# Performance work log

Measured on AMD Instinct MI355X. Metric: run time of the kernel, lower is better.

## Reference

```python
import jax, jax.numpy as jnp
import numpy as np

EMBED_DIM = 1024
HEADS = 16
D_HEAD = EMBED_DIM // HEADS
B, S = 4, 2048


def setup_inputs() -> dict:
    key = jax.random.key(0)
    ks = jax.random.split(key, 7)
    scale = 1.0 / np.sqrt(EMBED_DIM)
    inp = {
        "key": jax.random.normal(ks[0], (B, S, EMBED_DIM), jnp.float32),
        "query": jax.random.normal(ks[1], (B, S, EMBED_DIM), jnp.float32),
        "value": jax.random.normal(ks[2], (B, S, EMBED_DIM), jnp.float32),
        # causal boolean mask, broadcastable to [B, H, S, S]
        "mask": jnp.tril(jnp.ones((S, S), dtype=bool))[None, None, :, :] * jnp.ones((B, 1, 1, 1), dtype=bool),
        # nn.Linear weights, stored torch-style as [out_features, in_features]
        "Wq": jax.random.normal(ks[3], (EMBED_DIM, EMBED_DIM), jnp.float32) * scale,
        "Wk": jax.random.normal(ks[4], (EMBED_DIM, EMBED_DIM), jnp.float32) * scale,
        "Wv": jax.random.normal(ks[5], (EMBED_DIM, EMBED_DIM), jnp.float32) * scale,
        "Wo": jax.random.normal(ks[6], (EMBED_DIM, EMBED_DIM), jnp.float32) * scale,
    }
    return inp


def reference(key, query, value, mask, Wq, Wk, Wv, Wo):
    # projections (nn.Linear, bias=False): x @ W.T
    q = query @ Wq.T                                    # [B,S,E]
    k = key @ Wk.T
    v = value @ Wv.T
    # split heads -> [B,H,S,d]
    def split(x):
        return x.reshape(B, S, HEADS, D_HEAD).transpose(0, 2, 1, 3)
    q, k, v = split(q), split(k), split(v)
    # scaled dot-product scores [B,H,S,S]
    scores = jnp.einsum("bhqd,bhkd->bhqk", q, k) / np.sqrt(D_HEAD).astype(np.float32)
    scores = jnp.where(mask, scores, jnp.float32(-1e9))
    attn = jax.nn.softmax(scores, axis=-1)
    # attention output, merge heads
    out = jnp.einsum("bhqk,bhkd->bhqd", attn, v)        # [B,H,S,d]
    out = out.transpose(0, 2, 1, 3).reshape(B, S, EMBED_DIM)
    return out @ Wo.T
```

## Files before the change

### kernel.cpp

```cpp
#include <hip/hip_runtime.h>

#define SEQ 2048
#define EMBED 1024
#define DHEAD 64

typedef _Float16 h8 __attribute__((ext_vector_type(8)));
typedef _Float16 h4 __attribute__((ext_vector_type(4)));
typedef float f4 __attribute__((ext_vector_type(4)));
typedef unsigned int u32;

__device__ __forceinline__ void gload_lds16(const void* g, void* l) {
    __builtin_amdgcn_global_load_lds(
        (const __attribute__((address_space(1))) u32*)g,
        (__attribute__((address_space(3))) u32*)l, 16, 0, 0);
}

__device__ __forceinline__ h8 cvt8(f4 a, f4 b) {
    return (h8){ (_Float16)a[0], (_Float16)a[1], (_Float16)a[2], (_Float16)a[3],
                 (_Float16)b[0], (_Float16)b[1], (_Float16)b[2], (_Float16)b[3] };
}

__global__ __launch_bounds__(256) void cvt_w(
    const float* __restrict__ wq, const float* __restrict__ wk,
    const float* __restrict__ wv, const float* __restrict__ wo,
    _Float16* __restrict__ wq16, _Float16* __restrict__ wk16,
    _Float16* __restrict__ wv16, _Float16* __restrict__ wo16)
{
    int bid = blockIdx.x;
    int seg = bid >> 10;
    size_t base = (size_t)(bid & 1023) * 1024 + threadIdx.x * 4;
    const float* src = seg == 0 ? wq : seg == 1 ? wk : seg == 2 ? wv : wo;
    _Float16* dst = seg == 0 ? wq16 : seg == 1 ? wk16 : seg == 2 ? wv16 : wo16;
    float scale = (seg == 0) ? 0.18033688011112042f : 1.0f;
    float4 x = *(const float4*)(src + base);
    h4 y = { (_Float16)(x.x * scale), (_Float16)(x.y * scale),
             (_Float16)(x.z * scale), (_Float16)(x.w * scale) };
    *(h4*)(dst + base) = y;
}

template <bool A32, bool B32>
__device__ __forceinline__ void gemm_core_t(const void* Ap, const void* Wp,
                                            int m0, int n0, int tid,
                                            _Float16* As, _Float16* Bs, f4 acc[4][4])
{
    const int lane = tid & 63, wave = tid >> 6;
    const int t16 = lane & 15, quad = lane >> 4;
    const int wm = (wave >> 1) * 64, wn = (wave & 1) * 64;
    const int r0 = tid >> 2;
    const int c0 = (tid & 3) * 8;

    for (int k0 = 0; k0 < 1024; k0 += 32) {
        __syncthreads();
        f4 xa0, xa1, xa2, xa3, xb0, xb1, xb2, xb3;
        if constexpr (A32) {
            const float* ga = (const float*)Ap + (size_t)(m0 + r0) * 1024 + c0 + k0;
            xa0 = *(const f4*)ga;       xa1 = *(const f4*)(ga + 4);
            xa2 = *(const f4*)(ga + 65536); xa3 = *(const f4*)(ga + 65536 + 4);
        }
        if constexpr (B32) {
            const float* gb = (const float*)Wp + (size_t)(n0 + r0) * 1024 + c0 + k0;
            xb0 = *(const f4*)gb;       xb1 = *(const f4*)(gb + 4);
            xb2 = *(const f4*)(gb + 65536); xb3 = *(const f4*)(gb + 65536 + 4);
        }
        if constexpr (!A32) {
            const _Float16* ga = (const _Float16*)Ap + (size_t)(m0 + r0) * 1024 + c0 + k0;
            gload_lds16(ga, As + wave * 512);
            gload_lds16(ga + (size_t)64 * 1024, As + 2048 + wave * 512);
        }
        if constexpr (!B32) {
            const _Float16* gb = (const _Float16*)Wp + (size_t)(n0 + r0) * 1024 + c0 + k0;
            gload_lds16(gb, Bs + wave * 512);
            gload_lds16(gb + (size_t)64 * 1024, Bs + 2048 + wave * 512);
        }
        if constexpr (A32) {
            *(h8*)(As + tid * 8) = cvt8(xa0, xa1);
            *(h8*)(As + 2048 + tid * 8) = cvt8(xa2, xa3);
        }
        if constexpr (B32) {
            *(h8*)(Bs + tid * 8) = cvt8(xb0, xb1);
            *(h8*)(Bs + 2048 + tid * 8) = cvt8(xb2, xb3);
        }
        __syncthreads();
        h8 af[4], bf[4];
#pragma unroll
        for (int i = 0; i < 4; ++i)
            af[i] = *(const h8*)(As + (wm + i * 16 + t16) * 32 + quad * 8);
#pragma unroll
        for (int j = 0; j < 4; ++j)
            bf[j] = *(const h8*)(Bs + (wn + j * 16 + t16) * 32 + quad * 8);
#pragma unroll
        for (int i = 0; i < 4; ++i)
#pragma unroll
            for (int j = 0; j < 4; ++j)
                acc[i][j] = __builtin_amdgcn_mfma_f32_16x16x32_f16(af[i], bf[j], acc[i][j], 0, 0, 0);
    }
}

__global__ __launch_bounds__(256) void proj_qkv(
    const float* __restrict__ qf, const float* __restrict__ kf, const float* __restrict__ vf,
    const _Float16* __restrict__ Wq, const _Float16* __restrict__ Wk, const _Float16* __restrict__ Wv,
    _Float16* __restrict__ Qh, _Float16* __restrict__ Kh, _Float16* __restrict__ Vt)
{
    __shared__ _Float16 As[4096], Bs[4096];
    const int tid = threadIdx.x;
    const int z = blockIdx.z;
    int m0, n0;
    f4 acc[4][4];
    const f4 z4 = {0.f, 0.f, 0.f, 0.f};
#pragma unroll
    for (int i = 0; i < 4; ++i)
#pragma unroll
        for (int j = 0; j < 4; ++j) acc[i][j] = z4;

    if (z == 2) {
        m0 = blockIdx.y * 128; n0 = blockIdx.x * 128;
        gemm_core_t<false, true>(Wv, vf, m0, n0, tid, As, Bs, acc);
    } else if (z == 0) {
        m0 = blockIdx.x * 128; n0 = blockIdx.y * 128;
        gemm_core_t<true, false>(qf, Wq, m0, n0, tid, As, Bs, acc);
    } else {
        m0 = blockIdx.x * 128; n0 = blockIdx.y * 128;
        gemm_core_t<true, false>(kf, Wk, m0, n0, tid, As, Bs, acc);
    }

    const int lane = tid & 63, wave = tid >> 6;
    const int t16 = lane & 15, quad = lane >> 4;
    const int wm = (wave >> 1) * 64, wn = (wave & 1) * 64;
#pragma unroll
    for (int i = 0; i < 4; ++i)
#pragma unroll
        for (int j = 0; j < 4; ++j)
#pragma unroll
            for (int reg = 0; reg < 4; ++reg) {
                int gm = m0 + wm + i * 16 + quad * 4 + reg;
                int gn = n0 + wn + j * 16 + t16;
                float vv = acc[i][j][reg];
                if (z < 2) {
                    int b = gm >> 11, s = gm & 2047, h = gn >> 6, dd = gn & 63;
                    _Float16* dst = (z == 0) ? Qh : Kh;
                    dst[(((size_t)(b * 16 + h) * SEQ) + s) * DHEAD + dd] = (_Float16)vv;
                } else {
                    int h = gm >> 6, dd = gm & 63, b = gn >> 11, s = gn & 2047;
                    int jt = s >> 6, ks = s & 63;
                    int j4 = ks >> 4, quadv = (ks >> 2) & 3, regv = ks & 3;
                    int dt = dd >> 4, t16v = dd & 15;
                    size_t off = (size_t)(b * 16 + h) * (SEQ * DHEAD)
                               + (size_t)(jt * 8 + dt * 2 + (j4 >> 1)) * 512
                               + (quadv * 16 + t16v) * 8 + (j4 & 1) * 4 + regv;
                    Vt[off] = (_Float16)vv;
                }
            }
}

__global__ __launch_bounds__(256) void attn3(
    const _Float16* __restrict__ Qh, const _Float16* __restrict__ Kh,
    const _Float16* __restrict__ Vt, _Float16* __restrict__ Ob)
{
    __shared__ _Float16 Kbuf[2][8][512];
    __shared__ _Float16 Vbuf[2][8][512];

    const int tid = threadIdx.x;
    const int lane = tid & 63, wave = tid >> 6;
    const int t16 = lane & 15, quad = lane >> 4;
    const int bh = blockIdx.x;
    const int b = bh >> 4, h = bh & 15;
    const int qb = (gridDim.y - 1) - blockIdx.y;
    const int q0 = qb * 128;
    const int nqt = qb * 2 + 2;

    const _Float16* Qp = Qh + (size_t)bh * SEQ * DHEAD;
    const _Float16* Kp = Kh + (size_t)bh * SEQ * DHEAD;
    const _Float16* Vp = Vt + (size_t)bh * SEQ * DHEAD;

    const int qlo[2] = { q0 + wave * 32, q0 + wave * 32 + 16 };
    const int last0 = (qlo[0] + 15) >> 6;

    h8 qf[2][2];
#pragma unroll
    for (int qb2 = 0; qb2 < 2; ++qb2)
#pragma unroll
        for (int kc = 0; kc < 2; ++kc)
            qf[qb2][kc] = *(const h8*)(Qp + (size_t)(qlo[qb2] + t16) * 64 + kc * 32 + quad * 8);

    const _Float16* Kl = Kp + t16 * 64 + quad * 8;
    const _Float16* Vl = Vp + lane * 8;

#define STAGE(jt_, bufi)                                                                  \
    do {                                                                                  \
        if (wave < 2) {                                                                   \
            _Pragma("unroll")                                                             \
            for (int i_ = 0; i_ < 4; ++i_) {                                              \
                int g_ = wave * 4 + i_;                                                   \
                gload_lds16(Kl + (jt_) * 4096 + (g_ >> 1) * 1024 + (g_ & 1) * 32,         \
                            &Kbuf[bufi][g_][0]);                                          \
            }                                                                             \
        } else {                                                                          \
            _Pragma("unroll")                                                             \
            for (int i_ = 0; i_ < 4; ++i_) {                                              \
                int g_ = (wave - 2) * 4 + i_;                                             \
                gload_lds16(Vl + ((jt_) * 8 + g_) * 512, &Vbuf[bufi][g_][0]);             \
            }                                                                             \
        }                                                                                 \
    } while (0)

    STAGE(0, 0);
    __syncthreads();

    float mv[2] = {-1e30f, -1e30f};
    float lv[2] = {0.f, 0.f};
    f4 o_acc[2][4];
    const f4 z4 = {0.f, 0.f, 0.f, 0.f};
#pragma unroll
    for (int qb2 = 0; qb2 < 2; ++qb2)
#pragma unroll
        for (int dt = 0; dt < 4; ++dt) o_acc[qb2][dt] = z4;

    for (int jt = 0; jt < nqt; ++jt) {
        const int buf = jt & 1;
        if (jt + 1 < nqt) STAGE(jt + 1, buf ^ 1);

        if (jt <= last0) {
            f4 s0[4], s1[4];
#pragma unroll
            for (int j4 = 0; j4 < 4; ++j4) {
                h8 kfa = *(const h8*)(&Kbuf[buf][j4 * 2 + 0][lane * 8]);
                h8 kfb = *(const h8*)(&Kbuf[buf][j4 * 2 + 1][lane * 8]);
                s1[j4] = __builtin_amdgcn_mfma_f32_16x16x32_f16(kfa, qf[1][0], z4, 0, 0, 0);
                s1[j4] = __builtin_amdgcn_mfma_f32_16x16x32_f16(kfb, qf[1][1], s1[j4], 0, 0, 0);
                s0[j4] = __builtin_amdgcn_mfma_f32_16x16x32_f16(kfa, qf[0][0], z4, 0, 0, 0);
                s0[j4] = __builtin_amdgcn_mfma_f32_16x16x32_f16(kfb, qf[0][1], s0[j4], 0, 0, 0);
            }

            h4 pf0[4], pf1[4];
            auto softmax_frag = [&](f4* s, int qb2, h4* pf) {
                const int myq = qlo[qb2] + t16;
                if ((jt << 6) + 63 > qlo[qb2]) {
#pragma unroll
                    for (int j4 = 0; j4 < 4; ++j4)
#pragma unroll
                        for (int reg = 0; reg < 4; ++reg) {
                            int kk = (jt << 6) + j4 * 16 + quad * 4 + reg;
                            if (kk > myq) s[j4][reg] = -1e30f;
                        }
                }
                float mr = s[0][0];
#pragma unroll
                for (int j4 = 0; j4 < 4; ++j4)
#pragma unroll
                    for (int reg = 0; reg < 4; ++reg) mr = fmaxf(mr, s[j4][reg]);
                mr = fmaxf(mr, __shfl_xor(mr, 16, 64));
                mr = fmaxf(mr, __shfl_xor(mr, 32, 64));
                float mn = mv[qb2];
                if (__any(mr > mn + 8.0f)) {
                    mn = fmaxf(mn, mr);
                    float al = __builtin_amdgcn_exp2f(mv[qb2] - mn);
                    mv[qb2] = mn;
                    lv[qb2] *= al;
#pragma unroll
                    for (int dt = 0; dt < 4; ++dt)
#pragma unroll
                        for (int reg = 0; reg < 4; ++reg) o_acc[qb2][dt][reg] *= al;
                }
                float rs = 0.f;
#pragma unroll
                for (int j4 = 0; j4 < 4; ++j4) {
#pragma unroll
                    for (int reg = 0; reg < 4; ++reg) {
                        float p = __builtin_amdgcn_exp2f(s[j4][reg] - mn);
                        s[j4][reg] = p;
                        rs += p;
                    }
                    pf[j4] = (h4){ (_Float16)s[j4][0], (_Float16)s[j4][1],
                                   (_Float16)s[j4][2], (_Float16)s[j4][3] };
                }
                rs += __shfl_xor(rs, 16, 64);
                rs += __shfl_xor(rs, 32, 64);
                lv[qb2] += rs;
            };
            softmax_frag(s0, 0, pf0);
            softmax_frag(s1, 1, pf1);

#pragma unroll
            for (int dt = 0; dt < 4; ++dt) {
#pragma unroll
                for (int j4p = 0; j4p < 2; ++j4p) {
                    h8 v2 = *(const h8*)(&Vbuf[buf][dt * 2 + j4p][lane * 8]);
                    h4 vlo = __builtin_shufflevector(v2, v2, 0, 1, 2, 3);
                    h4 vhi = __builtin_shufflevector(v2, v2, 4, 5, 6, 7);
                    o_acc[0][dt] = __builtin_amdgcn_mfma_f32_16x16x16f16(vlo, pf0[j4p * 2 + 0], o_acc[0][dt], 0, 0, 0);
                    o_acc[0][dt] = __builtin_amdgcn_mfma_f32_16x16x16f16(vhi, pf0[j4p * 2 + 1], o_acc[0][dt], 0, 0, 0);
                    o_acc[1][dt] = __builtin_amdgcn_mfma_f32_16x16x16f16(vlo, pf1[j4p * 2 + 0], o_acc[1][dt], 0, 0, 0);
                    o_acc[1][dt] = __builtin_amdgcn_mfma_f32_16x16x16f16(vhi, pf1[j4p * 2 + 1], o_acc[1][dt], 0, 0, 0);
                }
            }
        }
        __syncthreads();
    }

    _Float16* ep = ((_Float16*)Kbuf) + wave * 1024;
    const int swz = (t16 & 7) << 3;
#pragma unroll
    for (int qb2 = 0; qb2 < 2; ++qb2) {
        float inv = __builtin_amdgcn_rcpf(lv[qb2]);
#pragma unroll
        for (int dt = 0; dt < 4; ++dt) {
            h4 ov = { (_Float16)(o_acc[qb2][dt][0] * inv), (_Float16)(o_acc[qb2][dt][1] * inv),
                      (_Float16)(o_acc[qb2][dt][2] * inv), (_Float16)(o_acc[qb2][dt][3] * inv) };
            *(h4*)(ep + t16 * 64 + ((dt * 16 + quad * 4) ^ swz)) = ov;
        }
        h8 r0 = *(const h8*)(ep + t16 * 64 + ((quad * 8) ^ swz));
        h8 r1 = *(const h8*)(ep + t16 * 64 + ((32 + quad * 8) ^ swz));
        int s = qlo[qb2] + t16;
        _Float16* og = Ob + ((size_t)(b * SEQ + s)) * EMBED + h * DHEAD;
        *(h8*)(og + quad * 8) = r0;
        *(h8*)(og + 32 + quad * 8) = r1;
    }
#undef STAGE
}

__global__ __launch_bounds__(256) void proj_out(
    const _Float16* __restrict__ A, const _Float16* __restrict__ Wo, float* __restrict__ out)
{
    __shared__ _Float16 As[4096], Bs[4096];
    const int tid = threadIdx.x;
    const int m0 = blockIdx.x * 128, n0 = blockIdx.y * 128;
    f4 acc[4][4];
    const f4 z4 = {0.f, 0.f, 0.f, 0.f};
#pragma unroll
    for (int i = 0; i < 4; ++i)
#pragma unroll
        for (int j = 0; j < 4; ++j) acc[i][j] = z4;

    gemm_core_t<false, false>(A, Wo, m0, n0, tid, As, Bs, acc);

    const int lane = tid & 63, wave = tid >> 6;
    const int t16 = lane & 15, quad = lane >> 4;
    const int wm = (wave >> 1) * 64, wn = (wave & 1) * 64;
#pragma unroll
    for (int i = 0; i < 4; ++i)
#pragma unroll
        for (int j = 0; j < 4; ++j)
#pragma unroll
            for (int reg = 0; reg < 4; ++reg) {
                int gm = m0 + wm + i * 16 + quad * 4 + reg;
                int gn = n0 + wn + j * 16 + t16;
                out[(size_t)gm * EMBED + gn] = acc[i][j][reg];
            }
}

extern "C" void kernel_launch(void* const* d_in, const int* in_sizes, int n_in,
                              void* d_out, int out_size, void* d_ws, size_t ws_size,
                              hipStream_t stream) {
    const float* key   = (const float*)d_in[0];
    const float* query = (const float*)d_in[1];
    const float* value = (const float*)d_in[2];
    const float* Wq = (const float*)d_in[4];
    const float* Wk = (const float*)d_in[5];
    const float* Wv = (const float*)d_in[6];
    const float* Wo = (const float*)d_in[7];

    char* ws = (char*)d_ws;
    _Float16* Ob   = (_Float16*)(ws);
    _Float16* Wq16 = (_Float16*)(ws + (16u << 20));
    _Float16* Wk16 = (_Float16*)(ws + (18u << 20));
    _Float16* Wv16 = (_Float16*)(ws + (20u << 20));
    _Float16* Wo16 = (_Float16*)(ws + (22u << 20));
    _Float16* Qh   = (_Float16*)(ws + (24u << 20));
    _Float16* Kh   = (_Float16*)(ws + (40u << 20));
    _Float16* Vt   = (_Float16*)(ws + (56u << 20));

    dim3 blk(256);
    cvt_w<<<dim3(4096), blk, 0, stream>>>(Wq, Wk, Wv, Wo, Wq16, Wk16, Wv16, Wo16);
    proj_qkv<<<dim3(64, 8, 3), blk, 0, stream>>>(query, key, value, Wq16, Wk16, Wv16, Qh, Kh, Vt);
    attn3<<<dim3(64, 16), blk, 0, stream>>>(Qh, Kh, Vt, Ob);
    proj_out<<<dim3(64, 8), blk, 0, stream>>>(Ob, Wo16, (float*)d_out);
}
```

Before: 364.9 us.

## Double-buffer LDS tiles in projection GEMM core to overlap loads with MFMA

Restructures the shared GEMM core used by the QKV and output projections into a two-stage pipeline. The next K-slice's global loads (direct-to-LDS for fp16, register prefetch for fp32) are issued before the current slice's MFMAs, and there is now one barrier per iteration instead of two. This is meant to hide global load latency behind compute. In exchange, LDS per block doubles to 32KB and fp32 operands stay live in registers across the MFMA section, which may reduce occupancy.

```diff
diff --git a/kernel.cpp b/kernel.cpp
--- a/kernel.cpp
+++ b/kernel.cpp
@@ -49,50 +49,74 @@
     const int r0 = tid >> 2;
     const int c0 = (tid & 3) * 8;
 
-    for (int k0 = 0; k0 < 1024; k0 += 32) {
-        __syncthreads();
-        f4 xa0, xa1, xa2, xa3, xb0, xb1, xb2, xb3;
+    f4 xa0, xa1, xa2, xa3, xb0, xb1, xb2, xb3;
+
+    auto loadA = [&](int k0, int bf) {
         if constexpr (A32) {
             const float* ga = (const float*)Ap + (size_t)(m0 + r0) * 1024 + c0 + k0;
-            xa0 = *(const f4*)ga;       xa1 = *(const f4*)(ga + 4);
+            xa0 = *(const f4*)ga;           xa1 = *(const f4*)(ga + 4);
             xa2 = *(const f4*)(ga + 65536); xa3 = *(const f4*)(ga + 65536 + 4);
-        }
+        } else {
+            const _Float16* ga = (const _Float16*)Ap + (size_t)(m0 + r0) * 1024 + c0 + k0;
+            gload_lds16(ga, As + bf * 4096 + wave * 512);
+            gload_lds16(ga + (size_t)64 * 1024, As + bf * 4096 + 2048 + wave * 512);
+        }
+    };
+    auto loadB = [&](int k0, int bf) {
         if constexpr (B32) {
             const float* gb = (const float*)Wp + (size_t)(n0 + r0) * 1024 + c0 + k0;
-            xb0 = *(const f4*)gb;       xb1 = *(const f4*)(gb + 4);
+            xb0 = *(const f4*)gb;           xb1 = *(const f4*)(gb + 4);
             xb2 = *(const f4*)(gb + 65536); xb3 = *(const f4*)(gb + 65536 + 4);
-        }
-        if constexpr (!A32) {
-            const _Float16* ga = (const _Float16*)Ap + (size_t)(m0 + r0) * 1024 + c0 + k0;
-            gload_lds16(ga, As + wave * 512);
-            gload_lds16(ga + (size_t)64 * 1024, As + 2048 + wave * 512);
-        }
-        if constexpr (!B32) {
+        } else {
             const _Float16* gb = (const _Float16*)Wp + (size_t)(n0 + r0) * 1024 + c0 + k0;
-            gload_lds16(gb, Bs + wave * 512);
-            gload_lds16(gb + (size_t)64 * 1024, Bs + 2048 + wave * 512);
-        }
+            gload_lds16(gb, Bs + bf * 4096 + wave * 512);
+            gload_lds16(gb + (size_t)64 * 1024, Bs + bf * 4096 + 2048 + wave * 512);
+        }
+    };
+    auto writeA = [&](int bf) {
         if constexpr (A32) {
-            *(h8*)(As + tid * 8) = cvt8(xa0, xa1);
-            *(h8*)(As + 2048 + tid * 8) = cvt8(xa2, xa3);
-        }
+            *(h8*)(As + bf * 4096 + tid * 8) = cvt8(xa0, xa1);
+            *(h8*)(As + bf * 4096 + 2048 + tid * 8) = cvt8(xa2, xa3);
+        }
+    };
+    auto writeB = [&](int bf) {
         if constexpr (B32) {
-            *(h8*)(Bs + tid * 8) = cvt8(xb0, xb1);
-            *(h8*)(Bs + 2048 + tid * 8) = cvt8(xb2, xb3);
+            *(h8*)(Bs + bf * 4096 + tid * 8) = cvt8(xb0, xb1);
+            *(h8*)(Bs + bf * 4096 + 2048 + tid * 8) = cvt8(xb2, xb3);
+        }
+    };
+
+    loadA(0, 0);
+    loadB(0, 0);
+    writeA(0);
+    writeB(0);
+    __syncthreads();
+
+    for (int k = 0; k < 32; ++k) {
+        const int b = k & 1;
+        if (k < 31) {
+            loadA((k + 1) * 32, b ^ 1);
+            loadB((k + 1) * 32, b ^ 1);
+        }
+        const _Float16* As_ = As + b * 4096;
+        const _Float16* Bs_ = Bs + b * 4096;
+        h8 af[4], bf4[4];
+#pragma unroll
+        for (int i = 0; i < 4; ++i)
+            af[i] = *(const h8*)(As_ + (wm + i * 16 + t16) * 32 + quad * 8);
+#pragma unroll
+        for (int j = 0; j < 4; ++j)
+            bf4[j] = *(const h8*)(Bs_ + (wn + j * 16 + t16) * 32 + quad * 8);
+#pragma unroll
+        for (int i = 0; i < 4; ++i)
+#pragma unroll
+            for (int j = 0; j < 4; ++j)
+                acc[i][j] = __builtin_amdgcn_mfma_f32_16x16x32_f16(af[i], bf4[j], acc[i][j], 0, 0, 0);
+        if (k < 31) {
+            writeA(b ^ 1);
+            writeB(b ^ 1);
         }
         __syncthreads();
-        h8 af[4], bf[4];
-#pragma unroll
-        for (int i = 0; i < 4; ++i)
-            af[i] = *(const h8*)(As + (wm + i * 16 + t16) * 32 + quad * 8);
-#pragma unroll
-        for (int j = 0; j < 4; ++j)
-            bf[j] = *(const h8*)(Bs + (wn + j * 16 + t16) * 32 + quad * 8);
-#pragma unroll
-        for (int i = 0; i < 4; ++i)
-#pragma unroll
-            for (int j = 0; j < 4; ++j)
-                acc[i][j] = __builtin_amdgcn_mfma_f32_16x16x32_f16(af[i], bf[j], acc[i][j], 0, 0, 0);
     }
 }
 
@@ -101,7 +125,7 @@
     const _Float16* __restrict__ Wq, const _Float16* __restrict__ Wk, const _Float16* __restrict__ Wv,
     _Float16* __restrict__ Qh, _Float16* __restrict__ Kh, _Float16* __restrict__ Vt)
 {
-    __shared__ _Float16 As[4096], Bs[4096];
+    __shared__ _Float16 As[8192], Bs[8192];
     const int tid = threadIdx.x;
     const int z = blockIdx.z;
     int m0, n0;
@@ -321,7 +345,7 @@
 __global__ __launch_bounds__(256) void proj_out(
     const _Float16* __restrict__ A, const _Float16* __restrict__ Wo, float* __restrict__ out)
 {
-    __shared__ _Float16 As[4096], Bs[4096];
+    __shared__ _Float16 As[8192], Bs[8192];
     const int tid = threadIdx.x;
     const int m0 = blockIdx.x * 128, n0 = blockIdx.y * 128;
     f4 acc[4][4];
```

New measurement: 362.7 us. No clear change (-0.6%).
